# Optimization experiments

Measured on AMD Instinct MI355X. Metric: run time of the kernel, lower is better.

## Reference

```python
import jax, jax.numpy as jnp
import numpy as np

STEP = 0.1  # step_size from init
H = 2048    # ceil(dim/2)


def setup_inputs() -> dict:
    key = jax.random.key(0)
    k1, k2, k3 = jax.random.split(key, 3)
    B, h = 16384, H
    x = jax.random.normal(k1, (B, 2 * h), dtype=jnp.float32)
    # Xavier-uniform-like scale for [2h, h] linear weights
    scale = (6.0 / (h + 2 * h)) ** 0.5
    W0 = jax.random.normal(k2, (2 * h, h), dtype=jnp.float32) * scale
    W1 = jax.random.normal(k3, (2 * h, h), dtype=jnp.float32) * scale
    b0 = jnp.zeros((2 * h,), dtype=jnp.float32)
    b1 = jnp.zeros((2 * h,), dtype=jnp.float32)
    return {"x": x, "W0": W0, "b0": b0, "W1": W1, "b1": b1}


def reference(x, W0, b0, W1, b1):
    h = W0.shape[1]
    u_old = x[:, :h]          # [B, h]
    v_old = x[:, h:]          # [B, h]
    # stage 1: Linear(u) -> tanh -> W1^T matmul -> scaled residual add
    v_mid = jnp.tanh(u_old @ W1.T + b1)   # [B, 2h]
    v_sig = v_mid @ W1                     # [B, h]  (tied-weight transpose matmul)
    v_new = v_old + STEP * v_sig
    # stage 2: Linear(v_new) -> tanh -> W0^T matmul -> scaled residual sub
    u_mid = jnp.tanh(v_new @ W0.T + b0)   # [B, 2h]
    u_sig = u_mid @ W0                     # [B, h]
    u_new = u_old - STEP * u_sig
    return jnp.concatenate((u_new, v_new), axis=1)
```

## Files before the change

kernel.cpp:

```cpp
#include <hip/hip_runtime.h>
#include <hip/hip_bf16.h>
#include <stdint.h>


typedef __attribute__((ext_vector_type(8))) short short8;
typedef __attribute__((ext_vector_type(4))) float f32x4;

#define DEVINL __device__ __forceinline__

DEVINL ushort f2b(float f) {
  union { float f; uint32_t u; } v; v.f = f;
  uint32_t u = v.u;
  return (ushort)((u + 0x7fffu + ((u >> 16) & 1u)) >> 16);
}

DEVINL float fast_tanh(float x) {
  x = fminf(10.0f, fmaxf(-10.0f, x));
  float e = __expf(2.0f * x);
  return (e - 1.0f) * __builtin_amdgcn_rcpf(e + 1.0f);
}

DEVINL void gload16(const ushort* g, ushort* l) {
  __builtin_amdgcn_global_load_lds(
      (const __attribute__((address_space(1))) void*)g,
      (__attribute__((address_space(3))) void*)l, 16, 0, 0);
}

template<int MH, int NH>
DEVINL void mfma_quad(f32x4 (&acc)[8][4], const short8 (&a)[4][2],
                      const short8 (&b)[2][2]) {
#pragma unroll
  for (int ks = 0; ks < 2; ++ks)
#pragma unroll
    for (int mi = 0; mi < 4; ++mi)
#pragma unroll
      for (int ni = 0; ni < 2; ++ni)
        acc[MH * 4 + mi][NH * 2 + ni] = __builtin_amdgcn_mfma_f32_16x16x32_bf16(
            a[mi][ks], b[ni][ks], acc[MH * 4 + mi][NH * 2 + ni], 0, 0, 0);
}

template<int MODE>
DEVINL void gemm_body(const ushort* __restrict__ A, const ushort* __restrict__ Bt,
                      const float* __restrict__ bias, ushort* __restrict__ Tout,
                      const float* __restrict__ xres, float* __restrict__ outres,
                      ushort* __restrict__ vbout, float step, int M, int N, int K)
{
  __shared__ __align__(16) ushort ldsU[32768];

  const int tid  = threadIdx.x;
  const int wave = tid >> 6, lane = tid & 63;
  const int wr = wave >> 2, wc = wave & 3;
  const int lr = lane & 15, hi = lane >> 4;

  const int GX = gridDim.x;
  const int nwg = GX * gridDim.y;
  const int lin = blockIdx.y * GX + blockIdx.x;
  const int swz = (lin & 7) * (nwg >> 3) + (lin >> 3);
  const int by = swz / GX, bx = swz - by * GX;
  const int m0 = by * 256, n0 = bx * 256;

  const int kb_st = ((tid & 7) * 16) ^ (((tid >> 3) & 7) << 4);
  int offA[2][2], offB[2][2];
#pragma unroll
  for (int j = 0; j < 2; ++j) {
    const int rp = j * 64 + (tid >> 3);
#pragma unroll
    for (int h = 0; h < 2; ++h) {
      offA[h][j] = (m0 + (rp >> 6) * 128 + h * 64 + (rp & 63)) * K + (kb_st >> 1);
      offB[h][j] = (n0 + (rp >> 5) * 64 + h * 32 + (rp & 31)) * K + (kb_st >> 1);
    }
  }

#define STAGE_A(half, t) do {                                                  \
    gload16(A + (size_t)offA[half][0] + (size_t)(t) * 64,                      \
            ldsU + (half) * 8192 + tid * 8);                                   \
    gload16(A + (size_t)offA[half][1] + (size_t)(t) * 64,                      \
            ldsU + (half) * 8192 + 4096 + tid * 8);                            \
  } while (0)
#define STAGE_B(half, t) do {                                                  \
    gload16(Bt + (size_t)offB[half][0] + (size_t)(t) * 64,                     \
            ldsU + 16384 + (half) * 8192 + tid * 8);                           \
    gload16(Bt + (size_t)offB[half][1] + (size_t)(t) * 64,                     \
            ldsU + 16384 + (half) * 8192 + 4096 + tid * 8);                    \
  } while (0)

  const int xm = (lane & 7) << 4;
  const int kbr0 = (hi * 16) ^ xm;
  const int kbr1 = (64 + hi * 16) ^ xm;
  const int eA0 = (wr * 64 + lr) * 64 + (kbr0 >> 1);
  const int eA1 = (wr * 64 + lr) * 64 + (kbr1 >> 1);
  const int eB0 = (wc * 32 + lr) * 64 + (kbr0 >> 1);
  const int eB1 = (wc * 32 + lr) * 64 + (kbr1 >> 1);

#define LDSE(idx) (*(const short8*)&ldsU[idx])
#define READ_A8(dst, half) do {                                                \
    dst[0][0] = LDSE((half)*8192 +    0 + eA0);                                \
    dst[0][1] = LDSE((half)*8192 +    0 + eA1);                                \
    dst[1][0] = LDSE((half)*8192 + 1024 + eA0);                                \
    dst[1][1] = LDSE((half)*8192 + 1024 + eA1);                                \
    dst[2][0] = LDSE((half)*8192 + 2048 + eA0);                                \
    dst[2][1] = LDSE((half)*8192 + 2048 + eA1);                                \
    dst[3][0] = LDSE((half)*8192 + 3072 + eA0);                                \
    dst[3][1] = LDSE((half)*8192 + 3072 + eA1);                                \
  } while (0)
#define READ_B4(dst, half) do {                                                \
    dst[0][0] = LDSE(16384 + (half)*8192 +    0 + eB0);                        \
    dst[0][1] = LDSE(16384 + (half)*8192 +    0 + eB1);                        \
    dst[1][0] = LDSE(16384 + (half)*8192 + 1024 + eB0);                        \
    dst[1][1] = LDSE(16384 + (half)*8192 + 1024 + eB1);                        \
  } while (0)

  f32x4 acc[8][4] = {};
  short8 a0[4][2], a1[4][2], b0[2][2], b1[2][2];

#define VMW(n) asm volatile("s_waitcnt vmcnt(" #n ")" ::: "memory")
#define LGK0 asm volatile("s_waitcnt lgkmcnt(0)" ::: "memory")
#define SCB __builtin_amdgcn_sched_barrier(0)
#define BAR __builtin_amdgcn_s_barrier()
#define PRIO1 __builtin_amdgcn_s_setprio(1)
#define PRIO0 __builtin_amdgcn_s_setprio(0)

  const int NT = K >> 6;

  STAGE_A(0, 0); STAGE_A(1, 0); STAGE_B(0, 0);
  STAGE_B(1, 0);
#pragma unroll 1
  for (int t = 0; t < NT - 1; ++t) {
    VMW(2); BAR; SCB;
    READ_A8(a0, 0); READ_B4(b0, 0); READ_A8(a1, 1);
    LGK0; SCB;
    BAR; SCB;
    STAGE_A(0, t + 1); STAGE_A(1, t + 1); STAGE_B(0, t + 1);
    PRIO1;
    mfma_quad<0, 0>(acc, a0, b0); mfma_quad<1, 0>(acc, a1, b0);
    PRIO0;
    VMW(6); BAR; SCB;
    READ_B4(b1, 1);
    LGK0; SCB;
    BAR; SCB;
    STAGE_B(1, t + 1);
    PRIO1;
    mfma_quad<0, 1>(acc, a0, b1); mfma_quad<1, 1>(acc, a1, b1);
    PRIO0;
  }
  VMW(2); BAR; SCB;
  READ_A8(a0, 0); READ_B4(b0, 0); READ_A8(a1, 1);
  LGK0; SCB;
  PRIO1;
  mfma_quad<0, 0>(acc, a0, b0); mfma_quad<1, 0>(acc, a1, b0);
  PRIO0;
  VMW(0); BAR; SCB;
  READ_B4(b1, 1);
  LGK0; SCB;
  PRIO1;
  mfma_quad<0, 1>(acc, a0, b1); mfma_quad<1, 1>(acc, a1, b1);
  PRIO0;

  const int mrow0 = m0 + wr * 128 + hi * 4;
  const int ncol0 = n0 + wc * 64 + lr;
#pragma unroll
  for (int mi = 0; mi < 8; ++mi) {
#pragma unroll
    for (int ni = 0; ni < 4; ++ni) {
      const int col = ncol0 + ni * 16;
      if (MODE == 0) {
        const float bv = bias[col];
#pragma unroll
        for (int r = 0; r < 4; ++r) {
          const int row = mrow0 + mi * 16 + r;
          Tout[(size_t)row * N + col] = f2b(fast_tanh(acc[mi][ni][r] + bv));
        }
      } else {
#pragma unroll
        for (int r = 0; r < 4; ++r) {
          const int row = mrow0 + mi * 16 + r;
          const size_t oi = (size_t)row * 4096 + col;
          const float v = fmaf(step, acc[mi][ni][r], xres[oi]);
          outres[oi] = v;
          if (MODE == 1) vbout[(size_t)row * N + col] = f2b(v);
        }
      }
    }
  }
#undef STAGE_A
#undef STAGE_B
#undef LDSE
#undef READ_A8
#undef READ_B4
#undef VMW
#undef LGK0
#undef SCB
#undef BAR
#undef PRIO1
#undef PRIO0
}

__global__ __launch_bounds__(512, 2)
void gemm_t1(const ushort* A, const ushort* Bt, const float* bias,
             ushort* Tout, int M, int N, int K) {
  gemm_body<0>(A, Bt, bias, Tout, nullptr, nullptr, nullptr, 0.f, M, N, K);
}
__global__ __launch_bounds__(512, 2)
void gemm_vnew(const ushort* A, const ushort* Bt, const float* xres,
               float* outres, ushort* vbout, float step, int M, int N, int K) {
  gemm_body<1>(A, Bt, nullptr, nullptr, xres, outres, vbout, step, M, N, K);
}
__global__ __launch_bounds__(512, 2)
void gemm_t2(const ushort* A, const ushort* Bt, const float* bias,
             ushort* Tout, int M, int N, int K) {
  gemm_body<0>(A, Bt, bias, Tout, nullptr, nullptr, nullptr, 0.f, M, N, K);
}
__global__ __launch_bounds__(512, 2)
void gemm_unew(const ushort* A, const ushort* Bt, const float* xres,
               float* outres, float step, int M, int N, int K) {
  gemm_body<2>(A, Bt, nullptr, nullptr, xres, outres, nullptr, step, M, N, K);
}

__global__ void cast_strided_half(const float* __restrict__ x,
                                  ushort* __restrict__ dst)
{
  const int i = blockIdx.x * blockDim.x + threadIdx.x;
  const int row = i >> 8;
  const int c8  = (i & 255) * 8;
  const float4 v0 = *(const float4*)&x[(size_t)row * 4096 + c8];
  const float4 v1 = *(const float4*)&x[(size_t)row * 4096 + c8 + 4];
  short8 o;
  o[0] = (short)f2b(v0.x); o[1] = (short)f2b(v0.y);
  o[2] = (short)f2b(v0.z); o[3] = (short)f2b(v0.w);
  o[4] = (short)f2b(v1.x); o[5] = (short)f2b(v1.y);
  o[6] = (short)f2b(v1.z); o[7] = (short)f2b(v1.w);
  *(short8*)&dst[(size_t)row * 2048 + c8] = o;
}

__global__ void pack_both(const float* __restrict__ W0, const float* __restrict__ W1,
                          ushort* __restrict__ W0b, ushort* __restrict__ W0t,
                          ushort* __restrict__ W1b, ushort* __restrict__ W1t)
{
  const float* W = blockIdx.z ? W1 : W0;
  ushort* Wb = blockIdx.z ? W1b : W0b;
  ushort* Wt = blockIdx.z ? W1t : W0t;
  __shared__ float tile[32][33];
  const int bx = blockIdx.x * 32;
  const int by = blockIdx.y * 32;
  const int tx = threadIdx.x, ty = threadIdx.y;
#pragma unroll
  for (int j = ty; j < 32; j += 8) {
    const float v = W[(size_t)(by + j) * 2048 + bx + tx];
    tile[j][tx] = v;
    Wb[(size_t)(by + j) * 2048 + bx + tx] = f2b(v);
  }
  __syncthreads();
#pragma unroll
  for (int j = ty; j < 32; j += 8) {
    Wt[(size_t)(bx + j) * 4096 + by + tx] = f2b(tile[tx][j]);
  }
}

extern "C" void kernel_launch(void* const* d_in, const int* in_sizes, int n_in,
                              void* d_out, int out_size, void* d_ws, size_t ws_size,
                              hipStream_t stream)
{
  const float* x  = (const float*)d_in[0];
  const float* W0 = (const float*)d_in[1];
  const float* b0 = (const float*)d_in[2];
  const float* W1 = (const float*)d_in[3];
  const float* b1 = (const float*)d_in[4];
  float* out = (float*)d_out;

  const int Mrows = 16384, H2 = 4096, Hh = 2048;

  uint8_t* ws = (uint8_t*)d_ws;
  ushort* T   = (ushort*)ws;
  ushort* Ab  = (ushort*)(ws + (size_t)134217728);
  ushort* W0b = (ushort*)(ws + (size_t)134217728 + 67108864);
  ushort* W0t = W0b + 8388608;
  ushort* W1b = W0t + 8388608;
  ushort* W1t = W1b + 8388608;

  cast_strided_half<<<16384, 256, 0, stream>>>(x, Ab);
  dim3 pw_grid(64, 128, 2), pw_blk(32, 8);
  pack_both<<<pw_grid, pw_blk, 0, stream>>>(W0, W1, W0b, W0t, W1b, W1t);

  dim3 blk(512);
  dim3 g1(H2 / 256, Mrows / 256);
  dim3 g2(Hh / 256, Mrows / 256);

  gemm_t1<<<g1, blk, 0, stream>>>(Ab, W1b, b1, T, Mrows, H2, Hh);
  gemm_vnew<<<g2, blk, 0, stream>>>(T, W1t, x + Hh, out + Hh, Ab, 0.1f,
                                    Mrows, Hh, H2);
  gemm_t2<<<g1, blk, 0, stream>>>(Ab, W0b, b0, T, Mrows, H2, Hh);
  gemm_unew<<<g2, blk, 0, stream>>>(T, W0t, x, out, -0.1f, Mrows, Hh, H2);
}
```

Measured before the change: 1.125 ms.

## Add double-buffered 128-deep K pipeline for stage-1 GEMMs

```diff
diff --git a/kernel.cpp b/kernel.cpp
--- a/kernel.cpp
+++ b/kernel.cpp
@@ -39,13 +39,14 @@
             a[mi][ks], b[ni][ks], acc[MH * 4 + mi][NH * 2 + ni], 0, 0, 0);
 }
 
-template<int MODE>
+template<int MODE, int SCHED>
 DEVINL void gemm_body(const ushort* __restrict__ A, const ushort* __restrict__ Bt,
                       const float* __restrict__ bias, ushort* __restrict__ Tout,
                       const float* __restrict__ xres, float* __restrict__ outres,
                       ushort* __restrict__ vbout, float step, int M, int N, int K)
 {
-  __shared__ __align__(16) ushort ldsU[32768];
+  constexpr int LDS_N = (SCHED == 7) ? 65536 : 32768;
+  __shared__ __align__(16) ushort ldsU[LDS_N];
 
   const int tid  = threadIdx.x;
   const int wave = tid >> 6, lane = tid & 63;
@@ -71,17 +72,34 @@
     }
   }
 
-#define STAGE_A(half, t) do {                                                  \
+#define STAGE_A3(half, t) do {                                                 \
     gload16(A + (size_t)offA[half][0] + (size_t)(t) * 64,                      \
             ldsU + (half) * 8192 + tid * 8);                                   \
     gload16(A + (size_t)offA[half][1] + (size_t)(t) * 64,                      \
             ldsU + (half) * 8192 + 4096 + tid * 8);                            \
   } while (0)
-#define STAGE_B(half, t) do {                                                  \
+#define STAGE_B3(half, t) do {                                                 \
     gload16(Bt + (size_t)offB[half][0] + (size_t)(t) * 64,                     \
             ldsU + 16384 + (half) * 8192 + tid * 8);                           \
     gload16(Bt + (size_t)offB[half][1] + (size_t)(t) * 64,                     \
             ldsU + 16384 + (half) * 8192 + 4096 + tid * 8);                    \
+  } while (0)
+
+#define STAGE_A7(kh, half, t) do {                                             \
+    gload16(A + (size_t)offA[half][0] + (size_t)(t) * 128 + (kh) * 64,         \
+            ldsU + (kh) * 16384 + (half) * 8192 + tid * 8);                    \
+    gload16(A + (size_t)offA[half][1] + (size_t)(t) * 128 + (kh) * 64,         \
+            ldsU + (kh) * 16384 + (half) * 8192 + 4096 + tid * 8);             \
+  } while (0)
+#define STAGE_B7(kh, half, t) do {                                             \
+    gload16(Bt + (size_t)offB[half][0] + (size_t)(t) * 128 + (kh) * 64,        \
+            ldsU + 32768 + (kh) * 16384 + (half) * 8192 + tid * 8);            \
+    gload16(Bt + (size_t)offB[half][1] + (size_t)(t) * 128 + (kh) * 64,        \
+            ldsU + 32768 + (kh) * 16384 + (half) * 8192 + 4096 + tid * 8);     \
+  } while (0)
+#define STAGE8_7(kh, t) do {                                                   \
+    STAGE_A7(kh, 0, t); STAGE_A7(kh, 1, t);                                    \
+    STAGE_B7(kh, 0, t); STAGE_B7(kh, 1, t);                                    \
   } while (0)
 
   const int xm = (lane & 7) << 4;
@@ -93,21 +111,21 @@
   const int eB1 = (wc * 32 + lr) * 64 + (kbr1 >> 1);
 
 #define LDSE(idx) (*(const short8*)&ldsU[idx])
-#define READ_A8(dst, half) do {                                                \
-    dst[0][0] = LDSE((half)*8192 +    0 + eA0);                                \
-    dst[0][1] = LDSE((half)*8192 +    0 + eA1);                                \
-    dst[1][0] = LDSE((half)*8192 + 1024 + eA0);                                \
-    dst[1][1] = LDSE((half)*8192 + 1024 + eA1);                                \
-    dst[2][0] = LDSE((half)*8192 + 2048 + eA0);                                \
-    dst[2][1] = LDSE((half)*8192 + 2048 + eA1);                                \
-    dst[3][0] = LDSE((half)*8192 + 3072 + eA0);                                \
-    dst[3][1] = LDSE((half)*8192 + 3072 + eA1);                                \
-  } while (0)
-#define READ_B4(dst, half) do {                                                \
-    dst[0][0] = LDSE(16384 + (half)*8192 +    0 + eB0);                        \
-    dst[0][1] = LDSE(16384 + (half)*8192 +    0 + eB1);                        \
-    dst[1][0] = LDSE(16384 + (half)*8192 + 1024 + eB0);                        \
-    dst[1][1] = LDSE(16384 + (half)*8192 + 1024 + eB1);                        \
+#define READ_A8(dst, base, half) do {                                          \
+    dst[0][0] = LDSE((base) + (half)*8192 +    0 + eA0);                       \
+    dst[0][1] = LDSE((base) + (half)*8192 +    0 + eA1);                       \
+    dst[1][0] = LDSE((base) + (half)*8192 + 1024 + eA0);                       \
+    dst[1][1] = LDSE((base) + (half)*8192 + 1024 + eA1);                       \
+    dst[2][0] = LDSE((base) + (half)*8192 + 2048 + eA0);                       \
+    dst[2][1] = LDSE((base) + (half)*8192 + 2048 + eA1);                       \
+    dst[3][0] = LDSE((base) + (half)*8192 + 3072 + eA0);                       \
+    dst[3][1] = LDSE((base) + (half)*8192 + 3072 + eA1);                       \
+  } while (0)
+#define READ_B4(dst, base, half) do {                                          \
+    dst[0][0] = LDSE((base) + (half)*8192 +    0 + eB0);                       \
+    dst[0][1] = LDSE((base) + (half)*8192 +    0 + eB1);                       \
+    dst[1][0] = LDSE((base) + (half)*8192 + 1024 + eB0);                       \
+    dst[1][1] = LDSE((base) + (half)*8192 + 1024 + eB1);                       \
   } while (0)
 
   f32x4 acc[8][4] = {};
@@ -120,41 +138,65 @@
 #define PRIO1 __builtin_amdgcn_s_setprio(1)
 #define PRIO0 __builtin_amdgcn_s_setprio(0)
 
-  const int NT = K >> 6;
-
-  STAGE_A(0, 0); STAGE_A(1, 0); STAGE_B(0, 0);
-  STAGE_B(1, 0);
+  if constexpr (SCHED == 7) {
+    const int NT = K >> 7;
+#define V7_PHASE(kh, STG, VN)                                                  \
+    VMW(VN); BAR; SCB;                                                         \
+    READ_A8(a0, (kh)*16384, 0); READ_B4(b0, 32768 + (kh)*16384, 0);            \
+    READ_A8(a1, (kh)*16384, 1); READ_B4(b1, 32768 + (kh)*16384, 1);            \
+    LGK0; SCB;                                                                 \
+    BAR; SCB;                                                                  \
+    STG;                                                                       \
+    PRIO1;                                                                     \
+    mfma_quad<0, 0>(acc, a0, b0); mfma_quad<1, 0>(acc, a1, b0);                \
+    mfma_quad<0, 1>(acc, a0, b1); mfma_quad<1, 1>(acc, a1, b1);                \
+    PRIO0;
+
+    STAGE8_7(0, 0); STAGE8_7(1, 0);
 #pragma unroll 1
-  for (int t = 0; t < NT - 1; ++t) {
+    for (int t = 0; t < NT - 1; ++t) {
+      V7_PHASE(0, STAGE8_7(0, t + 1), 8)
+      V7_PHASE(1, STAGE8_7(1, t + 1), 8)
+    }
+    V7_PHASE(0, , 8)
+    V7_PHASE(1, , 0)
+#undef V7_PHASE
+  } else {
+    const int NT = K >> 6;
+    STAGE_A3(0, 0); STAGE_A3(1, 0); STAGE_B3(0, 0);
+    STAGE_B3(1, 0);
+#pragma unroll 1
+    for (int t = 0; t < NT - 1; ++t) {
+      VMW(2); BAR; SCB;
+      READ_A8(a0, 0, 0); READ_B4(b0, 16384, 0); READ_A8(a1, 0, 1);
+      LGK0; SCB;
+      BAR; SCB;
+      STAGE_A3(0, t + 1); STAGE_A3(1, t + 1); STAGE_B3(0, t + 1);
+      PRIO1;
+      mfma_quad<0, 0>(acc, a0, b0); mfma_quad<1, 0>(acc, a1, b0);
+      PRIO0;
+      VMW(6); BAR; SCB;
+      READ_B4(b1, 16384, 1);
+      LGK0; SCB;
+      BAR; SCB;
+      STAGE_B3(1, t + 1);
+      PRIO1;
+      mfma_quad<0, 1>(acc, a0, b1); mfma_quad<1, 1>(acc, a1, b1);
+      PRIO0;
+    }
     VMW(2); BAR; SCB;
-    READ_A8(a0, 0); READ_B4(b0, 0); READ_A8(a1, 1);
+    READ_A8(a0, 0, 0); READ_B4(b0, 16384, 0); READ_A8(a1, 0, 1);
     LGK0; SCB;
-    BAR; SCB;
-    STAGE_A(0, t + 1); STAGE_A(1, t + 1); STAGE_B(0, t + 1);
     PRIO1;
     mfma_quad<0, 0>(acc, a0, b0); mfma_quad<1, 0>(acc, a1, b0);
     PRIO0;
-    VMW(6); BAR; SCB;
-    READ_B4(b1, 1);
+    VMW(0); BAR; SCB;
+    READ_B4(b1, 16384, 1);
     LGK0; SCB;
-    BAR; SCB;
-    STAGE_B(1, t + 1);
     PRIO1;
     mfma_quad<0, 1>(acc, a0, b1); mfma_quad<1, 1>(acc, a1, b1);
     PRIO0;
   }
-  VMW(2); BAR; SCB;
-  READ_A8(a0, 0); READ_B4(b0, 0); READ_A8(a1, 1);
-  LGK0; SCB;
-  PRIO1;
-  mfma_quad<0, 0>(acc, a0, b0); mfma_quad<1, 0>(acc, a1, b0);
-  PRIO0;
-  VMW(0); BAR; SCB;
-  READ_B4(b1, 1);
-  LGK0; SCB;
-  PRIO1;
-  mfma_quad<0, 1>(acc, a0, b1); mfma_quad<1, 1>(acc, a1, b1);
-  PRIO0;
 
   const int mrow0 = m0 + wr * 128 + hi * 4;
   const int ncol0 = n0 + wc * 64 + lr;
@@ -182,8 +224,11 @@
       }
     }
   }
-#undef STAGE_A
-#undef STAGE_B
+#undef STAGE_A3
+#undef STAGE_B3
+#undef STAGE_A7
+#undef STAGE_B7
+#undef STAGE8_7
 #undef LDSE
 #undef READ_A8
 #undef READ_B4
@@ -198,22 +243,22 @@
 __global__ __launch_bounds__(512, 2)
 void gemm_t1(const ushort* A, const ushort* Bt, const float* bias,
              ushort* Tout, int M, int N, int K) {
-  gemm_body<0>(A, Bt, bias, Tout, nullptr, nullptr, nullptr, 0.f, M, N, K);
+  gemm_body<0, 7>(A, Bt, bias, Tout, nullptr, nullptr, nullptr, 0.f, M, N, K);
 }
 __global__ __launch_bounds__(512, 2)
 void gemm_vnew(const ushort* A, const ushort* Bt, const float* xres,
                float* outres, ushort* vbout, float step, int M, int N, int K) {
-  gemm_body<1>(A, Bt, nullptr, nullptr, xres, outres, vbout, step, M, N, K);
+  gemm_body<1, 7>(A, Bt, nullptr, nullptr, xres, outres, vbout, step, M, N, K);
 }
 __global__ __launch_bounds__(512, 2)
 void gemm_t2(const ushort* A, const ushort* Bt, const float* bias,
              ushort* Tout, int M, int N, int K) {
-  gemm_body<0>(A, Bt, bias, Tout, nullptr, nullptr, nullptr, 0.f, M, N, K);
+  gemm_body<0, 3>(A, Bt, bias, Tout, nullptr, nullptr, nullptr, 0.f, M, N, K);
 }
 __global__ __launch_bounds__(512, 2)
 void gemm_unew(const ushort* A, const ushort* Bt, const float* xres,
                float* outres, float step, int M, int N, int K) {
-  gemm_body<2>(A, Bt, nullptr, nullptr, xres, outres, nullptr, step, M, N, K);
+  gemm_body<2, 3>(A, Bt, nullptr, nullptr, xres, outres, nullptr, step, M, N, K);
 }
 
 __global__ void cast_strided_half(const float* __restrict__ x,
```

Result: slower. 1.502 ms (+33.6%).
